# Kernel optimization log

Hardware: AMD Instinct MI355X
Metric: run time of the kernel (lower is better)

The kernel has to match this reference:

```python
import jax, jax.numpy as jnp
import numpy as np

B, C, N = 2, 256, 8192
H = W = 64
C4 = C // 4
EPS = 1e-5


def bn(x, gamma, beta, mean, var):
    # eval-mode batchnorm over channel axis 1
    shape = (1, -1) + (1,) * (x.ndim - 2)
    inv = gamma * jax.lax.rsqrt(var + EPS)
    return x * inv.reshape(shape) + (beta - mean * inv).reshape(shape)


def conv1x1(x, w, b):
    # w: (Cout, Cin)
    return jnp.einsum('bchw,oc->bohw', x, w) + b.reshape(1, -1, 1, 1)


def conv2d(x, w, b=None, padding='VALID', groups=1, lhs_dilation=None):
    y = jax.lax.conv_general_dilated(
        x, w, window_strides=(1, 1), padding=padding,
        lhs_dilation=lhs_dilation, feature_group_count=groups,
        dimension_numbers=('NCHW', 'OIHW', 'NCHW'))
    return y if b is None else y + b.reshape(1, -1, 1, 1)


def lift_net(x, w1, b1, w2, b2, axis):
    # DAWN predictor/updater: ReflectionPad(2,1) -> conv k=4 along axis (C4->2C4)
    # -> ReLU -> 1x1 conv (2C4->C4) -> Tanh
    pad = [(0, 0)] * 4
    pad[axis] = (2, 1)
    xp = jnp.pad(x, pad, mode='reflect')
    k = w1[:, :, None, :] if axis == 3 else w1[:, :, :, None]
    h = jax.nn.relu(conv2d(xp, k, b1))
    return jnp.tanh(conv1x1(h, w2, b2))


def lifting(x, pw, axis):
    # pw = (w1, b1, w2, b2), each with leading net axis [P, U]
    w1, b1, w2, b2 = pw
    sl_e = [slice(None)] * 4; sl_e[axis] = slice(0, None, 2)
    sl_o = [slice(None)] * 4; sl_o[axis] = slice(1, None, 2)
    x_even, x_odd = x[tuple(sl_e)], x[tuple(sl_o)]
    d = x_odd - lift_net(x_even, w1[0], b1[0], w2[0], b2[0], axis)
    c = x_even + lift_net(d, w1[1], b1[1], w2[1], b2[1], axis)
    return c, d


def wavelet2d(x, w1, b1, w2, b2):
    # leading axes of weights: (scheme[horizontal, vertical], net[P, U])
    c, d = lifting(x, (w1[0], b1[0], w2[0], b2[0]), axis=3)  # split along W
    v = (w1[1], b1[1], w2[1], b2[1])                          # shared vertical weights
    LL, LH = lifting(c, v, axis=2)
    HL, HH = lifting(d, v, axis=2)
    return LL, LH, HL, HH


def convT(x, w, b):
    # torch ConvTranspose2d(k=4, stride=2, pad=1); w: (Cin, Cout, 4, 4)
    wc = jnp.flip(w, (2, 3)).transpose(1, 0, 2, 3)  # (Cout, Cin, 4, 4)
    return conv2d(x, wc, b, padding=[(2, 2), (2, 2)], lhs_dilation=(2, 2))


def _forward(tokens, flatten_mat, bn_gamma, bn_beta, bn_mean, bn_var, red_w, red_b,
             lift_w1, lift_b1, lift_w2, lift_b2,
             ff2_w1, ff2_b1, ff2_w2, ff2_b2, ct2_w, ct2_b,
             bn2_gamma, bn2_beta, bn2_mean, bn2_var,
             ff1_w1, ff1_b1, ff1_w2, ff1_b2, ct1_w, ct1_b,
             bn1_gamma, bn1_beta, bn1_mean, bn1_var,
             dw1_w, dw1_b, dw2_w, dw2_b, scale_w, inflate_idx):
    r = bn(tokens, bn_gamma, bn_beta, bn_mean, bn_var)                       # (B,C,N)
    r = jnp.einsum('bmn,bcn->bcm', flatten_mat, r).reshape(B, C, H, W)       # flatten to grid
    rr = conv1x1(r, red_w, red_b)                                            # (B,C/4,H,W)
    LL1, LH1, HL1, HH1 = wavelet2d(rr, lift_w1[0], lift_b1[0], lift_w2[0], lift_b2[0])
    LL2, LH2, HL2, HH2 = wavelet2d(LL1, lift_w1[1], lift_b1[1], lift_w2[1], lift_b2[1])
    x2 = jnp.concatenate([LL2, LH2, HL2, HH2], 1)                            # (B,C,H/4,W/4)
    y2 = conv1x1(jax.nn.gelu(conv1x1(x2, ff2_w1, ff2_b1), approximate=False), ff2_w2, ff2_b2)
    y2 = bn(convT(y2, ct2_w, ct2_b), bn2_gamma, bn2_beta, bn2_mean, bn2_var) # (B,C/2,H/2,W/2)
    x1 = jnp.concatenate([LL1, LH1, HL1, HH1, y2], 1)                        # (B,1.5C,H/2,W/2)
    y1 = conv1x1(jax.nn.gelu(conv1x1(x1, ff1_w1, ff1_b1), approximate=False), ff1_w2, ff1_b2)
    y1 = bn(convT(y1, ct1_w, ct1_b), bn1_gamma, bn1_beta, bn1_mean, bn1_var) # (B,C,H,W)
    r = r + y1
    r = conv2d(r, dw1_w, dw1_b, padding=[(1, 1), (1, 1)], groups=C)          # depthwise 3x3
    r = conv2d(jax.nn.relu(r), dw2_w, dw2_b, padding=[(1, 1), (1, 1)], groups=C)
    r = r.reshape(B, C, H * W) * scale_w.reshape(1, C, 1)                    # grouped 1x1 conv1d
    r = jnp.take_along_axis(r, inflate_idx, axis=2)                          # inflate gather
    return tokens + r


def setup_inputs() -> dict:
    key = jax.random.key(0)
    ks = iter(jax.random.split(key, 64))
    nrm = lambda shape, s=0.05: jax.random.normal(next(ks), shape, jnp.float32) * s
    uni = lambda shape: jax.random.uniform(next(ks), shape, jnp.float32, 0.5, 1.5)
    return dict(
        tokens=jax.random.normal(next(ks), (B, C, N), jnp.float32),
        flatten_mat=nrm((B, H * W, N), 0.02),
        inflate_idx=jax.random.randint(next(ks), (B, C, N), 0, H * W),
        bn_gamma=jnp.ones((C,), jnp.float32), bn_beta=jnp.zeros((C,), jnp.float32),
        bn_mean=nrm((C,), 0.1), bn_var=uni((C,)),
        red_w=nrm((C4, C)), red_b=nrm((C4,)),
        lift_w1=nrm((2, 2, 2, 2 * C4, C4, 4)), lift_b1=nrm((2, 2, 2, 2 * C4)),
        lift_w2=nrm((2, 2, 2, C4, 2 * C4)), lift_b2=nrm((2, 2, 2, C4)),
        ff2_w1=nrm((C, C)), ff2_b1=nrm((C,)), ff2_w2=nrm((C, C)), ff2_b2=nrm((C,)),
        ct2_w=nrm((C, C // 2, 4, 4)), ct2_b=nrm((C // 2,)),
        bn2_gamma=jnp.ones((C // 2,), jnp.float32), bn2_beta=jnp.zeros((C // 2,), jnp.float32),
        bn2_mean=nrm((C // 2,), 0.1), bn2_var=uni((C // 2,)),
        ff1_w1=nrm((C, C + C // 2)), ff1_b1=nrm((C,)), ff1_w2=nrm((C, C)), ff1_b2=nrm((C,)),
        ct1_w=nrm((C, C, 4, 4)), ct1_b=nrm((C,)),
        bn1_gamma=jnp.ones((C,), jnp.float32), bn1_beta=jnp.zeros((C,), jnp.float32),
        bn1_mean=nrm((C,), 0.1), bn1_var=uni((C,)),
        dw1_w=nrm((C, 1, 3, 3)), dw1_b=nrm((C,)),
        dw2_w=nrm((C, 1, 3, 3)), dw2_b=nrm((C,)),
        scale_w=nrm((C,), 0.2),
    )


def reference(tokens, flatten_mat, inflate_idx, bn_gamma, bn_beta, bn_mean, bn_var,
              red_w, red_b, lift_w1, lift_b1, lift_w2, lift_b2,
              ff2_w1, ff2_b1, ff2_w2, ff2_b2, ct2_w, ct2_b,
              bn2_gamma, bn2_beta, bn2_mean, bn2_var,
              ff1_w1, ff1_b1, ff1_w2, ff1_b2, ct1_w, ct1_b,
              bn1_gamma, bn1_beta, bn1_mean, bn1_var,
              dw1_w, dw1_b, dw2_w, dw2_b, scale_w):
    return _forward(tokens, flatten_mat, bn_gamma, bn_beta, bn_mean, bn_var, red_w, red_b,
                    lift_w1, lift_b1, lift_w2, lift_b2,
                    ff2_w1, ff2_b1, ff2_w2, ff2_b2, ct2_w, ct2_b,
                    bn2_gamma, bn2_beta, bn2_mean, bn2_var,
                    ff1_w1, ff1_b1, ff1_w2, ff1_b2, ct1_w, ct1_b,
                    bn1_gamma, bn1_beta, bn1_mean, bn1_var,
                    dw1_w, dw1_b, dw2_w, dw2_b, scale_w, inflate_idx)
```

## Files before the change

### kernel.cpp

```cpp
#include <hip/hip_runtime.h>
#include <math.h>

#define EPSV 1e-5f

typedef __attribute__((ext_vector_type(8))) short bf16x8;
typedef __attribute__((ext_vector_type(4))) float f32x4;
typedef __attribute__((ext_vector_type(8))) unsigned short u16x8;

__device__ inline unsigned short f2bf(float f) {
    unsigned u = __float_as_uint(f);
    unsigned r = (u + 0x7fffu + ((u >> 16) & 1u)) >> 16;
    return (unsigned short)r;
}

__device__ inline void gload_lds16(const void* g, void* l) {
    __builtin_amdgcn_global_load_lds(
        (const __attribute__((address_space(1))) void*)g,
        (__attribute__((address_space(3))) void*)l, 16, 0, 0);
}

__global__ __launch_bounds__(256) void bn_to_bf16_kernel(
    const float4* __restrict__ x, ushort4* __restrict__ y,
    const float* __restrict__ g, const float* __restrict__ be,
    const float* __restrict__ mu, const float* __restrict__ va)
{
    int i = blockIdx.x * 256 + threadIdx.x;
    int c = (i >> 11) & 255;
    float s = g[c] * rsqrtf(va[c] + EPSV);
    float t = be[c] - mu[c] * s;
    float4 v = x[i];
    ushort4 h;
    h.x = f2bf(v.x * s + t); h.y = f2bf(v.y * s + t);
    h.z = f2bf(v.z * s + t); h.w = f2bf(v.w * s + t);
    y[i] = h;
}

__global__ __launch_bounds__(256) void flatten_gemm_mfma(
    const unsigned short* __restrict__ A, const float* __restrict__ Bm,
    float* __restrict__ Pbase)
{
    __shared__ __align__(16) unsigned short AS[4][256 * 32];
    __shared__ __align__(16) unsigned short BS[4][64 * 32];
    const int NTT = 64;
    int t = threadIdx.x;
    int wid = t >> 6, lane = t & 63;
    int n0 = blockIdx.x * 64;
    int ks = blockIdx.z & 3, b = blockIdx.z >> 2;
    const unsigned short* Ab = A + b * (256 * 8192);
    const float* Bb = Bm + (long)b * (4096 * 8192) + (long)n0 * 8192;
    int k0 = ks * 2048;
    int brow = t >> 3, bc8 = t & 7;
    int l15 = lane & 15, kc = lane >> 4;

    f32x4 acc[4][4] = {};

    auto issueA = [&](int tile, int buf) {
        int kb = k0 + tile * 32;
        #pragma unroll
        for (int j = 0; j < 4; ++j) {
            int d16 = (wid * 4 + j) * 64 + lane;
            int row = d16 >> 2;
            int ch = (d16 & 3) ^ ((row >> 1) & 3);
            gload_lds16(Ab + row * 8192 + kb + ch * 8, &AS[buf][(wid * 4 + j) * 512]);
        }
    };
    auto loadB = [&](int tile, float4& f0, float4& f1) {
        int kb = k0 + tile * 32;
        f0 = *(const float4*)(Bb + brow * 8192 + kb + bc8 * 4);
        f1 = *(const float4*)(Bb + (brow + 32) * 8192 + kb + bc8 * 4);
    };
    auto writeB = [&](int buf, const float4& f0, const float4& f1) {
        int ch16 = (bc8 >> 1) ^ ((brow >> 1) & 3);
        ushort4 h;
        h.x = f2bf(f0.x); h.y = f2bf(f0.y); h.z = f2bf(f0.z); h.w = f2bf(f0.w);
        *reinterpret_cast<ushort4*>(&BS[buf][brow * 32 + ch16 * 8 + (bc8 & 1) * 4]) = h;
        int rr2 = brow + 32;
        int ch16b = (bc8 >> 1) ^ ((rr2 >> 1) & 3);
        ushort4 h2;
        h2.x = f2bf(f1.x); h2.y = f2bf(f1.y); h2.z = f2bf(f1.z); h2.w = f2bf(f1.w);
        *reinterpret_cast<ushort4*>(&BS[buf][rr2 * 32 + ch16b * 8 + (bc8 & 1) * 4]) = h2;
    };
    auto mmac = [&](int buf) {
        bf16x8 af[4], bfr[4];
        #pragma unroll
        for (int mf = 0; mf < 4; ++mf) {
            int row = wid * 64 + mf * 16 + l15;
            int ch = kc ^ ((row >> 1) & 3);
            af[mf] = *reinterpret_cast<const bf16x8*>(&AS[buf][row * 32 + ch * 8]);
        }
        #pragma unroll
        for (int nf = 0; nf < 4; ++nf) {
            int row = nf * 16 + l15;
            int ch = kc ^ ((row >> 1) & 3);
            bfr[nf] = *reinterpret_cast<const bf16x8*>(&BS[buf][row * 32 + ch * 8]);
        }
        #pragma unroll
        for (int mf = 0; mf < 4; ++mf)
            #pragma unroll
            for (int nf = 0; nf < 4; ++nf)
                acc[mf][nf] = __builtin_amdgcn_mfma_f32_16x16x32_bf16(
                    af[mf], bfr[nf], acc[mf][nf], 0, 0, 0);
    };

    float4 p0, p1, e0, e1, q0, q1, r0, r1;
    loadB(0, p0, p1);
    loadB(1, e0, e1);
    loadB(2, q0, q1);
    issueA(0, 0); issueA(1, 1); issueA(2, 2);
    writeB(0, p0, p1);
    writeB(1, e0, e1);
    asm volatile("s_waitcnt vmcnt(8) lgkmcnt(0)" ::: "memory");
    __builtin_amdgcn_s_barrier();
    __builtin_amdgcn_sched_barrier(0);

    for (int tau = 0; tau < NTT; ++tau) {
        int cur = tau & 3;
        if (tau + 3 < NTT) {
            loadB(tau + 3, r0, r1);
            issueA(tau + 3, (tau + 3) & 3);
        }
        if (tau + 2 < NTT)
            writeB((tau + 2) & 3, q0, q1);
        mmac(cur);
        if (tau < NTT - 3)
            asm volatile("s_waitcnt vmcnt(8) lgkmcnt(0)" ::: "memory");
        else if (tau == NTT - 3)
            asm volatile("s_waitcnt vmcnt(4) lgkmcnt(0)" ::: "memory");
        else
            asm volatile("s_waitcnt vmcnt(0) lgkmcnt(0)" ::: "memory");
        __builtin_amdgcn_s_barrier();
        __builtin_amdgcn_sched_barrier(0);
        q0 = r0; q1 = r1;
    }

    float* P = Pbase + (long)ks * 2097152;
    float* Cb = P + (b * 256) * 4096 + n0;
    #pragma unroll
    for (int mf = 0; mf < 4; ++mf) {
        int rbase = wid * 64 + mf * 16 + (lane >> 4) * 4;
        #pragma unroll
        for (int nf = 0; nf < 4; ++nf) {
            int col = nf * 16 + (lane & 15);
            #pragma unroll
            for (int r = 0; r < 4; ++r)
                Cb[(rbase + r) * 4096 + col] = acc[mf][nf][r];
        }
    }
}

__global__ __launch_bounds__(256) void add4_t_kernel(
    const float* __restrict__ p, float* __restrict__ of32, unsigned short* __restrict__ obf)
{
    __shared__ float tl[64][65];
    int t = threadIdx.x;
    int b = blockIdx.z;
    int c0 = blockIdx.y * 64, p0 = blockIdx.x * 64;
    #pragma unroll
    for (int u = 0; u < 16; ++u) {
        int idx = u * 256 + t;
        int cl = idx >> 6, pl = idx & 63;
        long g = (long)(b * 256 + c0 + cl) * 4096 + p0 + pl;
        float v = p[g] + p[g + 2097152] + p[g + 2 * 2097152] + p[g + 3 * 2097152];
        tl[cl][pl] = v;
        of32[g] = v;
    }
    __syncthreads();
    #pragma unroll
    for (int u = 0; u < 16; ++u) {
        int idx = u * 256 + t;
        int pl = idx >> 6, cl = idx & 63;
        obf[(long)(b * 4096 + p0 + pl) * 256 + c0 + cl] = f2bf(tl[cl][pl]);
    }
}

__global__ __launch_bounds__(256) void wpack_kernel(
    const float* __restrict__ w, unsigned short* __restrict__ wp, int Cout, int Cin)
{
    int id = blockIdx.x * 256 + threadIdx.x;
    int nc8 = Cin >> 3;
    int cch = id % nc8;
    int rest = id / nc8;
    int o = rest % Cout;
    int pt = rest / Cout;
    if (pt >= 16) return;
    int par = pt >> 2, tap = pt & 3;
    int py = par >> 1, px = par & 1, u = tap >> 1, v = tap & 1;
    int tf = (3 - py - 2 * u) * 4 + (3 - px - 2 * v);
    u16x8 h;
    #pragma unroll
    for (int e = 0; e < 8; ++e)
        h[e] = f2bf(w[((cch * 8 + e) * Cout + o) * 16 + tf]);
    *reinterpret_cast<u16x8*>(&wp[((pt * Cout + o) * Cin) + cch * 8]) = h;
}

template<int NF>
__global__ __launch_bounds__(256) void conv1x1_mfma(
    const unsigned short* __restrict__ xbf, const float* __restrict__ w,
    const float* __restrict__ bias, float* __restrict__ of32,
    unsigned short* __restrict__ obf, int Cin, int Cout, int P, int act)
{
    constexpr int BP = NF * 64;
    __shared__ __align__(16) unsigned short XS[2][BP * 32];
    __shared__ __align__(16) unsigned short WS[2][64 * 32];
    int t = threadIdx.x;
    int wid = t >> 6, lane = t & 63;
    int b = blockIdx.z;
    int p0 = blockIdx.x * BP, o0 = blockIdx.y * 64;
    const unsigned short* xb = xbf + (long)b * P * Cin;
    int wm = t >> 2, wq = t & 3;
    int chunks = Cin >> 5;

    f32x4 acc[4][NF] = {};

    #pragma unroll
    for (int j = 0; j < NF; ++j) {
        int d16 = (wid * NF + j) * 64 + lane;
        int p = d16 >> 2;
        int ch = (d16 & 3) ^ ((p >> 1) & 3);
        gload_lds16(xb + (long)(p0 + p) * Cin + ch * 8, &XS[0][(wid * NF + j) * 512]);
    }
    float4 wr0 = *(const float4*)(w + (o0 + wm) * Cin + wq * 8);
    float4 wr1 = *(const float4*)(w + (o0 + wm) * Cin + wq * 8 + 4);
    __syncthreads();

    for (int cc = 0; cc < chunks; ++cc) {
        int cur = cc & 1;
        {
            int chq = wq ^ ((wm >> 1) & 3);
            u16x8 h;
            h[0] = f2bf(wr0.x); h[1] = f2bf(wr0.y); h[2] = f2bf(wr0.z); h[3] = f2bf(wr0.w);
            h[4] = f2bf(wr1.x); h[5] = f2bf(wr1.y); h[6] = f2bf(wr1.z); h[7] = f2bf(wr1.w);
            *reinterpret_cast<u16x8*>(&WS[cur][wm * 32 + chq * 8]) = h;
        }
        __syncthreads();

        if (cc < chunks - 1) {
            int kn = (cc + 1) * 32;
            #pragma unroll
            for (int j = 0; j < NF; ++j) {
                int d16 = (wid * NF + j) * 64 + lane;
                int p = d16 >> 2;
                int ch = (d16 & 3) ^ ((p >> 1) & 3);
                gload_lds16(xb + (long)(p0 + p) * Cin + kn + ch * 8,
                            &XS[cur ^ 1][(wid * NF + j) * 512]);
            }
            wr0 = *(const float4*)(w + (o0 + wm) * Cin + kn + wq * 8);
            wr1 = *(const float4*)(w + (o0 + wm) * Cin + kn + wq * 8 + 4);
        }

        int l15 = lane & 15, kc = lane >> 4;
        bf16x8 af[4], bfr[NF];
        #pragma unroll
        for (int mf = 0; mf < 4; ++mf) {
            int row = mf * 16 + l15;
            int ch = kc ^ ((row >> 1) & 3);
            af[mf] = *reinterpret_cast<const bf16x8*>(&WS[cur][row * 32 + ch * 8]);
        }
        #pragma unroll
        for (int nf = 0; nf < NF; ++nf) {
            int row = wid * (NF * 16) + nf * 16 + l15;
            int ch = kc ^ ((row >> 1) & 3);
            bfr[nf] = *reinterpret_cast<const bf16x8*>(&XS[cur][row * 32 + ch * 8]);
        }
        #pragma unroll
        for (int mf = 0; mf < 4; ++mf)
            #pragma unroll
            for (int nf = 0; nf < NF; ++nf)
                acc[mf][nf] = __builtin_amdgcn_mfma_f32_16x16x32_bf16(
                    af[mf], bfr[nf], acc[mf][nf], 0, 0, 0);
        __syncthreads();
    }

    int l15 = lane & 15, kc4 = lane >> 4;
    #pragma unroll
    for (int mf = 0; mf < 4; ++mf) {
        #pragma unroll
        for (int nf = 0; nf < NF; ++nf) {
            int p = wid * (NF * 16) + nf * 16 + l15;
            ushort4 hb;
            #pragma unroll
            for (int r = 0; r < 4; ++r) {
                int m = mf * 16 + kc4 * 4 + r;
                float v = acc[mf][nf][r] + bias[o0 + m];
                if (act == 1) v = fmaxf(v, 0.f);
                else if (act == 2) v = 0.5f * v * (1.f + erff(v * 0.70710678118f));
                if (of32) of32[((long)(b * Cout) + o0 + m) * P + p0 + p] = v;
                ((unsigned short*)&hb)[r] = f2bf(v);
            }
            if (obf)
                *reinterpret_cast<ushort4*>(
                    &obf[(long)(b * P + p0 + p) * Cout + o0 + mf * 16 + kc4 * 4]) = hb;
        }
    }
}

__global__ __launch_bounds__(256) void convt_mfma(
    const unsigned short* __restrict__ xbf, const unsigned short* __restrict__ wp,
    const float* __restrict__ bias, const float* __restrict__ g,
    const float* __restrict__ be, const float* __restrict__ mu,
    const float* __restrict__ va, const float* __restrict__ res,
    float* __restrict__ of32, unsigned short* __restrict__ obf,
    int Cin, int Cout, int Hin, int Win, int TR, int cshift, int OCtot, int cof)
{
    __shared__ __align__(16) unsigned short XS[165 * 32];
    __shared__ __align__(16) unsigned short WS[4 * 64 * 32];
    int t = threadIdx.x;
    int wid = t >> 6, lane = t & 63;
    int z = blockIdx.z;
    int b = z >> 2, par = z & 3;
    int py = par >> 1, px = par & 1;
    int o0 = blockIdx.y * 64;
    int i0 = blockIdx.x * TR;
    int CW = Win, CW1 = CW + 1;
    int npatch = (TR + 1) * CW1;
    int Pin = Hin * Win, Pout = 4 * Hin * Win;
    const unsigned short* xb = xbf + (long)b * Pin * Cin;
    int chunks = Cin >> 5;
    int l15 = lane & 15, kc = lane >> 4;

    f32x4 acc[4][2] = {};

    for (int cc = 0; cc < chunks; ++cc) {
        __syncthreads();
        for (int idx = t; idx < npatch * 4; idx += 256) {
            int pp = idx >> 2, ql = idx & 3;
            int qs = ql ^ ((pp >> 1) & 3);
            int a = pp / CW1, bcol = pp - a * CW1;
            int iy = i0 - (1 - py) + a;
            int ix = bcol - (1 - px);
            u16x8 v = {};
            if (iy >= 0 && iy < Hin && ix >= 0 && ix < Win)
                v = *reinterpret_cast<const u16x8*>(
                    &xb[(long)(iy * Win + ix) * Cin + cc * 32 + qs * 8]);
            *reinterpret_cast<u16x8*>(&XS[pp * 32 + ql * 8]) = v;
        }
        {
            int m = t >> 2, q = t & 3;
            int chq = q ^ ((m >> 1) & 3);
            #pragma unroll
            for (int tap = 0; tap < 4; ++tap) {
                u16x8 v = *reinterpret_cast<const u16x8*>(
                    &wp[((long)((par * 4 + tap) * Cout + o0 + m)) * Cin + cc * 32 + q * 8]);
                *reinterpret_cast<u16x8*>(&WS[tap * 2048 + m * 32 + chq * 8]) = v;
            }
        }
        __syncthreads();

        #pragma unroll
        for (int tap = 0; tap < 4; ++tap) {
            int u = tap >> 1, v = tap & 1;
            bf16x8 af[4], bfr[2];
            #pragma unroll
            for (int mf = 0; mf < 4; ++mf) {
                int row = mf * 16 + l15;
                int ch = kc ^ ((row >> 1) & 3);
                af[mf] = *reinterpret_cast<const bf16x8*>(&WS[tap * 2048 + row * 32 + ch * 8]);
            }
            #pragma unroll
            for (int nf = 0; nf < 2; ++nf) {
                int n = wid * 32 + nf * 16 + l15;
                int rn = n >> cshift, cn = n & (CW - 1);
                int pp = (rn + u) * CW1 + cn + v;
                int ch = kc ^ ((pp >> 1) & 3);
                bfr[nf] = *reinterpret_cast<const bf16x8*>(&XS[pp * 32 + ch * 8]);
            }
            #pragma unroll
            for (int mf = 0; mf < 4; ++mf)
                #pragma unroll
                for (int nf = 0; nf < 2; ++nf)
                    acc[mf][nf] = __builtin_amdgcn_mfma_f32_16x16x32_bf16(
                        af[mf], bfr[nf], acc[mf][nf], 0, 0, 0);
        }
    }

    int kc4 = lane >> 4;
    #pragma unroll
    for (int nf = 0; nf < 2; ++nf) {
        int n = wid * 32 + nf * 16 + l15;
        int rn = n >> cshift, cn = n & (CW - 1);
        int y = 2 * (i0 + rn) + py;
        int xx = 2 * cn + px;
        int pout = y * 2 * Win + xx;
        #pragma unroll
        for (int mf = 0; mf < 4; ++mf) {
            ushort4 hb;
            #pragma unroll
            for (int r = 0; r < 4; ++r) {
                int m = mf * 16 + kc4 * 4 + r;
                int o = o0 + m;
                float s = g[o] * rsqrtf(va[o] + EPSV);
                float v = (acc[mf][nf][r] + bias[o]) * s + (be[o] - mu[o] * s);
                if (res) v += res[((long)(b * Cout) + o) * Pout + pout];
                if (of32) of32[((long)(b * Cout) + o) * Pout + pout] = v;
                ((unsigned short*)&hb)[r] = f2bf(v);
            }
            if (obf)
                *reinterpret_cast<ushort4*>(
                    &obf[(long)(b * Pout + pout) * OCtot + cof + o0 + mf * 16 + kc4 * 4]) = hb;
        }
    }
}

__global__ __launch_bounds__(1024) void lift_net_kernel(
    const float* __restrict__ xA, const float* __restrict__ xB,
    const float* __restrict__ oA, const float* __restrict__ oB,
    float* __restrict__ uA, float* __restrict__ uB,
    int x_sB, int x_sC, int x_sR, int x_sA,
    int o_sB, int o_sC, int o_sR, int o_sA,
    int u_sB, int u_sC, int u_sR, int u_sA,
    const float* __restrict__ w1, const float* __restrict__ b1,
    const float* __restrict__ w2, const float* __restrict__ b2,
    int R, int L, int lsh, float sign,
    unsigned short* __restrict__ obf, int Pb, int OCb, int cofA, int cofB)
{
    __shared__ float xsm[4864];
    __shared__ float hsm[8192];
    int t = threadIdx.x;
    int g = t & 63, ocg = t >> 6;
    int b = blockIdx.z;
    int sel = blockIdx.y;
    const float* xin = sel ? xB : xA;
    const float* oth = sel ? oB : oA;
    float* outp = sel ? uB : uA;
    int cofb = sel ? cofB : cofA;
    int rpb = 64 >> lsh;
    int row0 = blockIdx.x * rpb;
    int Lp = L + 3;
    int total = 64 * rpb * Lp;
    for (int idx = t; idx < total; idx += 1024) {
        int c = idx / (rpb * Lp);
        int rem = idx - c * rpb * Lp;
        int rr_l = rem / Lp;
        int q = rem - rr_l * Lp;
        int s = q - 2;
        s = (s < 0) ? -s : s;
        if (s >= L) s = 2 * L - 2 - s;
        xsm[idx] = xin[b * x_sB + c * x_sC + (row0 + rr_l) * x_sR + s * x_sA];
    }
    __syncthreads();

    int ocgu = __builtin_amdgcn_readfirstlane(ocg);
    int rl = g >> lsh, jl = g & (L - 1);
    const float* w1u = w1 + ocgu * 8 * 256;
    float acc1[8] = {};
    for (int c = 0; c < 64; ++c) {
        const float* xr = &xsm[(c * rpb + rl) * Lp + jl];
        float x0 = xr[0], x1 = xr[1], x2 = xr[2], x3 = xr[3];
        const float* wc = w1u + c * 4;
        #pragma unroll
        for (int k = 0; k < 8; ++k) {
            const float* wr = wc + k * 256;
            acc1[k] += wr[0] * x0 + wr[1] * x1 + wr[2] * x2 + wr[3] * x3;
        }
    }
    #pragma unroll
    for (int k = 0; k < 8; ++k) {
        int oc = ocgu * 8 + k;
        hsm[oc * 64 + g] = fmaxf(acc1[k] + b1[oc], 0.f);
    }
    __syncthreads();

    const float* w2u = w2 + ocgu * 4 * 128;
    float acc2[4] = {};
    for (int h4 = 0; h4 < 32; ++h4) {
        float hv0 = hsm[(h4 * 4 + 0) * 64 + g];
        float hv1 = hsm[(h4 * 4 + 1) * 64 + g];
        float hv2 = hsm[(h4 * 4 + 2) * 64 + g];
        float hv3 = hsm[(h4 * 4 + 3) * 64 + g];
        #pragma unroll
        for (int kk = 0; kk < 4; ++kk) {
            const float* wr = w2u + kk * 128 + h4 * 4;
            acc2[kk] += wr[0] * hv0 + wr[1] * hv1 + wr[2] * hv2 + wr[3] * hv3;
        }
    }
    int rg = row0 + rl;
    int p = rg * u_sR + jl * u_sA;
    #pragma unroll
    for (int kk = 0; kk < 4; ++kk) {
        int o = ocgu * 4 + kk;
        float v = oth[b * o_sB + o * o_sC + rg * o_sR + jl * o_sA]
                + sign * tanhf(acc2[kk] + b2[o]);
        outp[b * u_sB + o * u_sC + p] = v;
        if (obf) obf[(long)(b * Pb + p) * OCb + cofb + o] = f2bf(v);
    }
}

__global__ __launch_bounds__(256) void dw_fused_kernel(
    const float* __restrict__ r2, const float* __restrict__ w1, const float* __restrict__ b1,
    const float* __restrict__ w2, const float* __restrict__ b2v,
    const float* __restrict__ scw, const float* __restrict__ tok,
    const int* __restrict__ idx, float* __restrict__ out)
{
    __shared__ float s0[64][68];
    __shared__ float s1[64][68];
    __shared__ float s2[4096];
    int bc = blockIdx.x;
    int c = bc & 255;
    int t = threadIdx.x;
    const float* xp = r2 + (long)bc * 4096;
    for (int i = t; i < 4096; i += 256) s0[i >> 6][i & 63] = xp[i];
    float wa[9], wb[9];
    #pragma unroll
    for (int k = 0; k < 9; ++k) { wa[k] = w1[c * 9 + k]; wb[k] = w2[c * 9 + k]; }
    float ba = b1[c], bb = b2v[c], sc = scw[c];
    __syncthreads();
    for (int i = t; i < 4096; i += 256) {
        int y = i >> 6, x = i & 63;
        float a = ba;
        #pragma unroll
        for (int ky = 0; ky < 3; ++ky) {
            int yy = y + ky - 1;
            if (yy < 0 || yy > 63) continue;
            #pragma unroll
            for (int kx = 0; kx < 3; ++kx) {
                int xx = x + kx - 1;
                if (xx < 0 || xx > 63) continue;
                a += wa[ky * 3 + kx] * s0[yy][xx];
            }
        }
        s1[y][x] = fmaxf(a, 0.f);
    }
    __syncthreads();
    for (int i = t; i < 4096; i += 256) {
        int y = i >> 6, x = i & 63;
        float a = bb;
        #pragma unroll
        for (int ky = 0; ky < 3; ++ky) {
            int yy = y + ky - 1;
            if (yy < 0 || yy > 63) continue;
            #pragma unroll
            for (int kx = 0; kx < 3; ++kx) {
                int xx = x + kx - 1;
                if (xx < 0 || xx > 63) continue;
                a += wb[ky * 3 + kx] * s1[yy][xx];
            }
        }
        s2[i] = a * sc;
    }
    __syncthreads();
    long base = (long)bc << 13;
    const int4* ip = (const int4*)(idx + base);
    const float4* tp = (const float4*)(tok + base);
    float4* op = (float4*)(out + base);
    for (int i = t; i < 2048; i += 256) {
        int4 iv = ip[i];
        float4 tv = tp[i];
        float4 o;
        o.x = tv.x + s2[iv.x];
        o.y = tv.y + s2[iv.y];
        o.z = tv.z + s2[iv.z];
        o.w = tv.w + s2[iv.w];
        op[i] = o;
    }
}

extern "C" void kernel_launch(void* const* d_in, const int* in_sizes, int n_in,
                              void* d_out, int out_size, void* d_ws, size_t ws_size,
                              hipStream_t stream)
{
    const float* tokens = (const float*)d_in[0];
    const float* fm     = (const float*)d_in[1];
    const int*   infl   = (const int*)d_in[2];
    const float* bng = (const float*)d_in[3];
    const float* bnb = (const float*)d_in[4];
    const float* bnm = (const float*)d_in[5];
    const float* bnv = (const float*)d_in[6];
    const float* red_w = (const float*)d_in[7];
    const float* red_b = (const float*)d_in[8];
    const float* lw1 = (const float*)d_in[9];
    const float* lb1 = (const float*)d_in[10];
    const float* lw2 = (const float*)d_in[11];
    const float* lb2 = (const float*)d_in[12];
    const float* f2w1 = (const float*)d_in[13];
    const float* f2b1 = (const float*)d_in[14];
    const float* f2w2 = (const float*)d_in[15];
    const float* f2b2 = (const float*)d_in[16];
    const float* ct2w = (const float*)d_in[17];
    const float* ct2b = (const float*)d_in[18];
    const float* bn2g = (const float*)d_in[19];
    const float* bn2b = (const float*)d_in[20];
    const float* bn2m = (const float*)d_in[21];
    const float* bn2v = (const float*)d_in[22];
    const float* f1w1 = (const float*)d_in[23];
    const float* f1b1 = (const float*)d_in[24];
    const float* f1w2 = (const float*)d_in[25];
    const float* f1b2 = (const float*)d_in[26];
    const float* ct1w = (const float*)d_in[27];
    const float* ct1b = (const float*)d_in[28];
    const float* bn1g = (const float*)d_in[29];
    const float* bn1b = (const float*)d_in[30];
    const float* bn1m = (const float*)d_in[31];
    const float* bn1v = (const float*)d_in[32];
    const float* dw1w = (const float*)d_in[33];
    const float* dw1b = (const float*)d_in[34];
    const float* dw2w = (const float*)d_in[35];
    const float* dw2b = (const float*)d_in[36];
    const float* scw  = (const float*)d_in[37];

    float* ws = (float*)d_ws;
    unsigned short* Abf = (unsigned short*)ws;
    float* part  = ws + 2097152;
    float* rgrid = ws + 18874368;
    unsigned short* rgrid_bf = (unsigned short*)(ws + 20971520);
    float* rr    = ws + 22020096;
    float* c1    = ws + 22544384;
    float* d1    = ws + 22806528;
    float* c2    = ws + 23068672;
    float* d2    = ws + 23134208;
    float* x2    = ws + 23199744;
    unsigned short* x2_bf  = (unsigned short*)(ws + 23330816);
    float* x1    = ws + 23396352;
    unsigned short* x1_bf  = (unsigned short*)(ws + 24182784);
    unsigned short* g2_bf  = (unsigned short*)(ws + 24576000);
    unsigned short* y2p_bf = (unsigned short*)(ws + 24641536);
    unsigned short* g1_bf  = (unsigned short*)(ws + 24707072);
    unsigned short* y1p_bf = (unsigned short*)(ws + 24969216);
    unsigned short* wp2    = (unsigned short*)(ws + 25231360);
    unsigned short* wp1    = (unsigned short*)(ws + 25493504);
    float* r2 = ws + 26017792;

    wpack_kernel<<<512, 256, 0, stream>>>(ct1w, wp1, 256, 256);
    wpack_kernel<<<256, 256, 0, stream>>>(ct2w, wp2, 128, 256);

    bn_to_bf16_kernel<<<4096, 256, 0, stream>>>((const float4*)tokens, (ushort4*)Abf,
                                                bng, bnb, bnm, bnv);
    flatten_gemm_mfma<<<dim3(64, 1, 8), 256, 0, stream>>>(Abf, fm, part);
    add4_t_kernel<<<dim3(64, 4, 2), 256, 0, stream>>>(part, rgrid, rgrid_bf);
    conv1x1_mfma<2><<<dim3(32, 1, 2), 256, 0, stream>>>(rgrid_bf, red_w, red_b,
                                                        rr, (unsigned short*)nullptr,
                                                        256, 64, 4096, 0);

    auto lift2 = [&](const float* xA, const float* xB, const float* oA, const float* oB,
                     float* uA, float* uB,
                     int xsB, int xsC, int xsR, int xsA,
                     int osB, int osC, int osR, int osA,
                     int usB, int usC, int usR, int usA,
                     int lvl, int sch, int net, int R, int L, float sign,
                     unsigned short* obf, int Pb, int OCb, int cofA, int cofB, int nsel) {
        int widx = (lvl * 2 + sch) * 2 + net;
        int lsh = (L == 32) ? 5 : 4;
        lift_net_kernel<<<dim3(R * L / 64, nsel, 2), 1024, 0, stream>>>(
            xA, xB, oA, oB, uA, uB,
            xsB, xsC, xsR, xsA, osB, osC, osR, osA, usB, usC, usR, usA,
            lw1 + widx * 32768, lb1 + widx * 128, lw2 + widx * 8192, lb2 + widx * 64,
            R, L, lsh, sign, obf, Pb, OCb, cofA, cofB);
    };

    lift2(rr, rr, rr + 1, rr + 1, d1, d1,
          262144, 4096, 64, 2,  262144, 4096, 64, 2,  131072, 2048, 32, 1,
          0, 0, 0, 64, 32, -1.f, nullptr, 0, 0, 0, 0, 1);
    lift2(d1, d1, rr, rr, c1, c1,
          131072, 2048, 32, 1,  262144, 4096, 64, 2,  131072, 2048, 32, 1,
          0, 0, 1, 64, 32, +1.f, nullptr, 0, 0, 0, 0, 1);
    lift2(c1, d1, c1 + 32, d1 + 32, x1 + 65536, x1 + 196608,
          131072, 2048, 1, 64,  131072, 2048, 1, 64,  393216, 1024, 1, 32,
          0, 1, 0, 32, 32, -1.f, x1_bf, 1024, 384, 64, 192, 2);
    lift2(x1 + 65536, x1 + 196608, c1, d1, x1, x1 + 131072,
          393216, 1024, 1, 32,  131072, 2048, 1, 64,  393216, 1024, 1, 32,
          0, 1, 1, 32, 32, +1.f, x1_bf, 1024, 384, 0, 128, 2);
    lift2(x1, x1, x1 + 1, x1 + 1, d2, d2,
          393216, 1024, 32, 2,  393216, 1024, 32, 2,  65536, 512, 16, 1,
          1, 0, 0, 32, 16, -1.f, nullptr, 0, 0, 0, 0, 1);
    lift2(d2, d2, x1, x1, c2, c2,
          65536, 512, 16, 1,  393216, 1024, 32, 2,  65536, 512, 16, 1,
          1, 0, 1, 32, 16, +1.f, nullptr, 0, 0, 0, 0, 1);
    lift2(c2, d2, c2 + 16, d2 + 16, x2 + 16384, x2 + 49152,
          65536, 512, 1, 32,  65536, 512, 1, 32,  65536, 256, 1, 16,
          1, 1, 0, 16, 16, -1.f, x2_bf, 256, 256, 64, 192, 2);
    lift2(x2 + 16384, x2 + 49152, c2, d2, x2, x2 + 32768,
          65536, 256, 1, 16,  65536, 512, 1, 32,  65536, 256, 1, 16,
          1, 1, 1, 16, 16, +1.f, x2_bf, 256, 256, 0, 128, 2);

    conv1x1_mfma<1><<<dim3(4, 4, 2), 256, 0, stream>>>(x2_bf, f2w1, f2b1,
        (float*)nullptr, g2_bf, 256, 256, 256, 2);
    conv1x1_mfma<1><<<dim3(4, 4, 2), 256, 0, stream>>>(g2_bf, f2w2, f2b2,
        (float*)nullptr, y2p_bf, 256, 256, 256, 0);
    convt_mfma<<<dim3(2, 2, 8), 256, 0, stream>>>(y2p_bf, wp2, ct2b,
        bn2g, bn2b, bn2m, bn2v, (const float*)nullptr,
        (float*)nullptr, x1_bf, 256, 128, 16, 16, 8, 4, 384, 256);

    conv1x1_mfma<2><<<dim3(8, 4, 2), 256, 0, stream>>>(x1_bf, f1w1, f1b1,
        (float*)nullptr, g1_bf, 384, 256, 1024, 2);
    conv1x1_mfma<2><<<dim3(8, 4, 2), 256, 0, stream>>>(g1_bf, f1w2, f1b2,
        (float*)nullptr, y1p_bf, 256, 256, 1024, 0);
    convt_mfma<<<dim3(8, 4, 8), 256, 0, stream>>>(y1p_bf, wp1, ct1b,
        bn1g, bn1b, bn1m, bn1v, rgrid,
        r2, (unsigned short*)nullptr, 256, 256, 32, 32, 4, 5, 0, 0);

    dw_fused_kernel<<<512, 256, 0, stream>>>(r2, dw1w, dw1b, dw2w, dw2b, scw,
                                             tokens, infl, (float*)d_out);
}
```

Baseline: 671.4 us.

## Rework flatten GEMM pipeline, remap block order, use bf16 residual grid

```diff
diff --git a/kernel.cpp b/kernel.cpp
--- a/kernel.cpp
+++ b/kernel.cpp
@@ -11,6 +11,10 @@
     unsigned u = __float_as_uint(f);
     unsigned r = (u + 0x7fffu + ((u >> 16) & 1u)) >> 16;
     return (unsigned short)r;
+}
+
+__device__ inline float bf2f(unsigned short h) {
+    return __uint_as_float(((unsigned)h) << 16);
 }
 
 __device__ inline void gload_lds16(const void* g, void* l) {
@@ -44,8 +48,11 @@
     const int NTT = 64;
     int t = threadIdx.x;
     int wid = t >> 6, lane = t & 63;
-    int n0 = blockIdx.x * 64;
-    int ks = blockIdx.z & 3, b = blockIdx.z >> 2;
+    int fid = blockIdx.z * 64 + blockIdx.x;
+    int nid = (fid & 7) * 64 + (fid >> 3);
+    int n0 = (nid & 63) * 64;
+    int zz = nid >> 6;
+    int ks = zz & 3, b = zz >> 2;
     const unsigned short* Ab = A + b * (256 * 8192);
     const float* Bb = Bm + (long)b * (4096 * 8192) + (long)n0 * 8192;
     int k0 = ks * 2048;
@@ -54,7 +61,8 @@
 
     f32x4 acc[4][4] = {};
 
-    auto issueA = [&](int tile, int buf) {
+    auto issueA = [&](int tile) {
+        int buf = tile & 3;
         int kb = k0 + tile * 32;
         #pragma unroll
         for (int j = 0; j < 4; ++j) {
@@ -69,7 +77,8 @@
         f0 = *(const float4*)(Bb + brow * 8192 + kb + bc8 * 4);
         f1 = *(const float4*)(Bb + (brow + 32) * 8192 + kb + bc8 * 4);
     };
-    auto writeB = [&](int buf, const float4& f0, const float4& f1) {
+    auto writeB = [&](int tile, const float4& f0, const float4& f1) {
+        int buf = tile & 3;
         int ch16 = (bc8 >> 1) ^ ((brow >> 1) & 3);
         ushort4 h;
         h.x = f2bf(f0.x); h.y = f2bf(f0.y); h.z = f2bf(f0.z); h.w = f2bf(f0.w);
@@ -80,7 +89,8 @@
         h2.x = f2bf(f1.x); h2.y = f2bf(f1.y); h2.z = f2bf(f1.z); h2.w = f2bf(f1.w);
         *reinterpret_cast<ushort4*>(&BS[buf][rr2 * 32 + ch16b * 8 + (bc8 & 1) * 4]) = h2;
     };
-    auto mmac = [&](int buf) {
+    auto mmac = [&](int tile) {
+        int buf = tile & 3;
         bf16x8 af[4], bfr[4];
         #pragma unroll
         for (int mf = 0; mf < 4; ++mf) {
@@ -102,35 +112,27 @@
                     af[mf], bfr[nf], acc[mf][nf], 0, 0, 0);
     };
 
-    float4 p0, p1, e0, e1, q0, q1, r0, r1;
-    loadB(0, p0, p1);
-    loadB(1, e0, e1);
-    loadB(2, q0, q1);
-    issueA(0, 0); issueA(1, 1); issueA(2, 2);
-    writeB(0, p0, p1);
-    writeB(1, e0, e1);
-    asm volatile("s_waitcnt vmcnt(8) lgkmcnt(0)" ::: "memory");
-    __builtin_amdgcn_s_barrier();
-    __builtin_amdgcn_sched_barrier(0);
+    float4 q00, q01, q10, q11, r0, r1;
+    loadB(0, q00, q01);
+    loadB(1, q10, q11);
+    issueA(0);
+    issueA(1);
 
     for (int tau = 0; tau < NTT; ++tau) {
-        int cur = tau & 3;
-        if (tau + 3 < NTT) {
-            loadB(tau + 3, r0, r1);
-            issueA(tau + 3, (tau + 3) & 3);
-        }
-        if (tau + 2 < NTT)
-            writeB((tau + 2) & 3, q0, q1);
-        mmac(cur);
-        if (tau < NTT - 3)
-            asm volatile("s_waitcnt vmcnt(8) lgkmcnt(0)" ::: "memory");
-        else if (tau == NTT - 3)
+        writeB(tau, q00, q01);
+        if (tau == 0)
             asm volatile("s_waitcnt vmcnt(4) lgkmcnt(0)" ::: "memory");
+        else if (tau < NTT - 1)
+            asm volatile("s_waitcnt vmcnt(6) lgkmcnt(0)" ::: "memory");
         else
             asm volatile("s_waitcnt vmcnt(0) lgkmcnt(0)" ::: "memory");
         __builtin_amdgcn_s_barrier();
-        __builtin_amdgcn_sched_barrier(0);
-        q0 = r0; q1 = r1;
+        if (tau + 2 < NTT) {
+            loadB(tau + 2, r0, r1);
+            issueA(tau + 2);
+        }
+        mmac(tau);
+        q00 = q10; q01 = q11; q10 = r0; q11 = r1;
     }
 
     float* P = Pbase + (long)ks * 2097152;
@@ -149,7 +151,7 @@
 }
 
 __global__ __launch_bounds__(256) void add4_t_kernel(
-    const float* __restrict__ p, float* __restrict__ of32, unsigned short* __restrict__ obf)
+    const float* __restrict__ p, unsigned short* __restrict__ obf)
 {
     __shared__ float tl[64][65];
     int t = threadIdx.x;
@@ -160,9 +162,7 @@
         int idx = u * 256 + t;
         int cl = idx >> 6, pl = idx & 63;
         long g = (long)(b * 256 + c0 + cl) * 4096 + p0 + pl;
-        float v = p[g] + p[g + 2097152] + p[g + 2 * 2097152] + p[g + 3 * 2097152];
-        tl[cl][pl] = v;
-        of32[g] = v;
+        tl[cl][pl] = p[g] + p[g + 2097152] + p[g + 2 * 2097152] + p[g + 3 * 2097152];
     }
     __syncthreads();
     #pragma unroll
@@ -298,7 +298,7 @@
     const unsigned short* __restrict__ xbf, const unsigned short* __restrict__ wp,
     const float* __restrict__ bias, const float* __restrict__ g,
     const float* __restrict__ be, const float* __restrict__ mu,
-    const float* __restrict__ va, const float* __restrict__ res,
+    const float* __restrict__ va, const unsigned short* __restrict__ resbf,
     float* __restrict__ of32, unsigned short* __restrict__ obf,
     int Cin, int Cout, int Hin, int Win, int TR, int cshift, int OCtot, int cof)
 {
@@ -390,7 +390,7 @@
                 int o = o0 + m;
                 float s = g[o] * rsqrtf(va[o] + EPSV);
                 float v = (acc[mf][nf][r] + bias[o]) * s + (be[o] - mu[o] * s);
-                if (res) v += res[((long)(b * Cout) + o) * Pout + pout];
+                if (resbf) v += bf2f(resbf[(long)(b * Pout + pout) * 256 + o]);
                 if (of32) of32[((long)(b * Cout) + o) * Pout + pout] = v;
                 ((unsigned short*)&hb)[r] = f2bf(v);
             }
@@ -600,24 +600,23 @@
     float* ws = (float*)d_ws;
     unsigned short* Abf = (unsigned short*)ws;
     float* part  = ws + 2097152;
-    float* rgrid = ws + 18874368;
-    unsigned short* rgrid_bf = (unsigned short*)(ws + 20971520);
-    float* rr    = ws + 22020096;
-    float* c1    = ws + 22544384;
-    float* d1    = ws + 22806528;
-    float* c2    = ws + 23068672;
-    float* d2    = ws + 23134208;
-    float* x2    = ws + 23199744;
-    unsigned short* x2_bf  = (unsigned short*)(ws + 23330816);
-    float* x1    = ws + 23396352;
-    unsigned short* x1_bf  = (unsigned short*)(ws + 24182784);
-    unsigned short* g2_bf  = (unsigned short*)(ws + 24576000);
-    unsigned short* y2p_bf = (unsigned short*)(ws + 24641536);
-    unsigned short* g1_bf  = (unsigned short*)(ws + 24707072);
-    unsigned short* y1p_bf = (unsigned short*)(ws + 24969216);
-    unsigned short* wp2    = (unsigned short*)(ws + 25231360);
-    unsigned short* wp1    = (unsigned short*)(ws + 25493504);
-    float* r2 = ws + 26017792;
+    unsigned short* rgrid_bf = (unsigned short*)(ws + 10485760);
+    float* rr    = ws + 11534336;
+    float* c1    = ws + 12058624;
+    float* d1    = ws + 12320768;
+    float* c2    = ws + 12582912;
+    float* d2    = ws + 12648448;
+    float* x2    = ws + 12713984;
+    unsigned short* x2_bf  = (unsigned short*)(ws + 12845056);
+    float* x1    = ws + 12910592;
+    unsigned short* x1_bf  = (unsigned short*)(ws + 13697024);
+    unsigned short* g2_bf  = (unsigned short*)(ws + 14090240);
+    unsigned short* y2p_bf = (unsigned short*)(ws + 14155776);
+    unsigned short* g1_bf  = (unsigned short*)(ws + 14221312);
+    unsigned short* y1p_bf = (unsigned short*)(ws + 14483456);
+    unsigned short* wp2    = (unsigned short*)(ws + 14745600);
+    unsigned short* wp1    = (unsigned short*)(ws + 15007744);
+    float* r2 = ws + 15532032;
 
     wpack_kernel<<<512, 256, 0, stream>>>(ct1w, wp1, 256, 256);
     wpack_kernel<<<256, 256, 0, stream>>>(ct2w, wp2, 128, 256);
@@ -625,7 +624,7 @@
     bn_to_bf16_kernel<<<4096, 256, 0, stream>>>((const float4*)tokens, (ushort4*)Abf,
                                                 bng, bnb, bnm, bnv);
     flatten_gemm_mfma<<<dim3(64, 1, 8), 256, 0, stream>>>(Abf, fm, part);
-    add4_t_kernel<<<dim3(64, 4, 2), 256, 0, stream>>>(part, rgrid, rgrid_bf);
+    add4_t_kernel<<<dim3(64, 4, 2), 256, 0, stream>>>(part, rgrid_bf);
     conv1x1_mfma<2><<<dim3(32, 1, 2), 256, 0, stream>>>(rgrid_bf, red_w, red_b,
                                                         rr, (unsigned short*)nullptr,
                                                         256, 64, 4096, 0);
@@ -676,7 +675,7 @@
     conv1x1_mfma<1><<<dim3(4, 4, 2), 256, 0, stream>>>(g2_bf, f2w2, f2b2,
         (float*)nullptr, y2p_bf, 256, 256, 256, 0);
     convt_mfma<<<dim3(2, 2, 8), 256, 0, stream>>>(y2p_bf, wp2, ct2b,
-        bn2g, bn2b, bn2m, bn2v, (const float*)nullptr,
+        bn2g, bn2b, bn2m, bn2v, (const unsigned short*)nullptr,
         (float*)nullptr, x1_bf, 256, 128, 16, 16, 8, 4, 384, 256);
 
     conv1x1_mfma<2><<<dim3(8, 4, 2), 256, 0, stream>>>(x1_bf, f1w1, f1b1,
@@ -684,7 +683,7 @@
     conv1x1_mfma<2><<<dim3(8, 4, 2), 256, 0, stream>>>(g1_bf, f1w2, f1b2,
         (float*)nullptr, y1p_bf, 256, 256, 1024, 0);
     convt_mfma<<<dim3(8, 4, 8), 256, 0, stream>>>(y1p_bf, wp1, ct1b,
-        bn1g, bn1b, bn1m, bn1v, rgrid,
+        bn1g, bn1b, bn1m, bn1v, rgrid_bf,
         r2, (unsigned short*)nullptr, 256, 256, 32, 32, 4, 5, 0, 0);
 
     dw_fused_kernel<<<512, 256, 0, stream>>>(r2, dw1w, dw1b, dw2w, dw2b, scw,
```

After: 660.0 us. No clear change (-1.7%).
